# Kernel optimization log

Hardware: AMD Instinct MI355X
Metric: run time of the kernel (lower is better)

The kernel has to match this reference:

```python
import jax, jax.numpy as jnp
import numpy as np

N = 50000
E = 1600000
D_IN = 128
D_OUT = 128


def setup_inputs() -> dict:
    key = jax.random.key(0)
    k1, k2, k3, k4, k5, k6 = jax.random.split(key, 6)
    row = jax.random.randint(k1, (E,), 0, N, dtype=jnp.int32)
    col = jax.random.randint(k2, (E,), 0, N, dtype=jnp.int32)
    vals = jax.random.uniform(k3, (E,), dtype=jnp.float32)
    features = jax.random.normal(k4, (N, D_IN), dtype=jnp.float32)
    weight = jax.random.normal(k5, (D_IN, D_OUT), dtype=jnp.float32)
    bias = jax.random.normal(k6, (D_OUT,), dtype=jnp.float32)
    return {"row": row, "col": col, "vals": vals, "features": features,
            "weight": weight, "bias": bias}


def reference(row, col, vals, features, weight, bias):
    # SpMM aggregation: out[i] = sum_j adj[i,j] * features[j]
    # adj given in COO: (row, col, vals)
    gathered = vals[:, None] * features[col]          # [E, D_IN]
    agg = jax.ops.segment_sum(gathered, row, num_segments=N)  # [N, D_IN]
    # dense feature transform + bias
    return agg @ weight + bias                        # [N, D_OUT]
```

## Files before the change

### kernel.cpp

```cpp
#include <hip/hip_runtime.h>
#include <hip/hip_bf16.h>


#define D 128
#define NREP 8
#define RPB 128
#define BCAP 5120
#define EPB 4096
#define NBMAX 512

typedef __attribute__((ext_vector_type(8))) short short8;
typedef __attribute__((ext_vector_type(4))) float f32x4;

__device__ __forceinline__ ushort bf16bits(float x) {
    return __hip_bfloat16_raw(__float2bfloat16(x)).x;
}

__global__ __launch_bounds__(256) void transposeW_k(const float* __restrict__ W,
                                                    ushort* __restrict__ Wt) {
    const int idx = blockIdx.x * 256 + threadIdx.x;
    const int k = idx >> 7, c = idx & 127;
    Wt[c * D + k] = bf16bits(W[idx]);
}

__global__ __launch_bounds__(256) void gemm_mfma_k(
    const float* __restrict__ F, const ushort* __restrict__ Wt,
    ushort* __restrict__ Gb, int nrows) {
    const int wave = threadIdx.x >> 6;
    const int lane = threadIdx.x & 63;
    const int row0 = (blockIdx.x * 4 + wave) * 16;
    if (row0 >= nrows) return;
    const int lr = lane & 15;
    const int lg = lane >> 4;

    f32x4 acc[8];
    #pragma unroll
    for (int c = 0; c < 8; ++c) acc[c] = (f32x4){0.f, 0.f, 0.f, 0.f};

    int arow_idx = row0 + lr;
    if (arow_idx >= nrows) arow_idx = nrows - 1;
    const float* __restrict__ arow = F + (size_t)arow_idx * D + lg * 8;

    #pragma unroll
    for (int kk = 0; kk < 4; ++kk) {
        const float4 a0 = *(const float4*)(arow + kk * 32);
        const float4 a1 = *(const float4*)(arow + kk * 32 + 4);
        short8 af;
        af[0] = (short)bf16bits(a0.x); af[1] = (short)bf16bits(a0.y);
        af[2] = (short)bf16bits(a0.z); af[3] = (short)bf16bits(a0.w);
        af[4] = (short)bf16bits(a1.x); af[5] = (short)bf16bits(a1.y);
        af[6] = (short)bf16bits(a1.z); af[7] = (short)bf16bits(a1.w);
        #pragma unroll
        for (int c = 0; c < 8; ++c) {
            const short8 bf = *(const short8*)(Wt + (size_t)(c * 16 + lr) * D + kk * 32 + lg * 8);
            acc[c] = __builtin_amdgcn_mfma_f32_16x16x32_bf16(af, bf, acc[c], 0, 0, 0);
        }
    }

    ushort* __restrict__ gout = Gb + (size_t)row0 * D;
    #pragma unroll
    for (int i = 0; i < 4; ++i) {
        const int r = 4 * lg + i;
        if (row0 + r < nrows) {
            #pragma unroll
            for (int c = 0; c < 8; ++c) {
                const int j = c * 16 + lr;
                const int pos = (c < 4) ? (2 * j) : (2 * (j - 64) + 1);
                gout[(size_t)r * D + pos] = bf16bits(acc[c][i]);
            }
        }
    }
}

__global__ __launch_bounds__(256) void bucket_scatter_k(
    const int* __restrict__ row, const int* __restrict__ col,
    const float* __restrict__ vals, int* __restrict__ gcur,
    uint2* __restrict__ pairs, int E, int NB) {
    __shared__ int hist[NBMAX];
    __shared__ int cur[NBMAX];
    const int t = threadIdx.x;
    for (int i = t; i < NB; i += 256) hist[i] = 0;
    __syncthreads();

    const int e0 = blockIdx.x * EPB;
    const int e1 = min(e0 + EPB, E);

    for (int e = e0 + t; e < e1; e += 256)
        atomicAdd(&hist[row[e] >> 7], 1);
    __syncthreads();

    for (int i = t; i < NB; i += 256) {
        const int h = hist[i];
        cur[i] = (h > 0) ? atomicAdd(&gcur[i], h) : 0;
    }
    __syncthreads();

    for (int e = e0 + t; e < e1; e += 256) {
        const int r = row[e];
        const int b = r >> 7;
        const int slot = atomicAdd(&cur[b], 1);
        if (slot < BCAP)
            pairs[(size_t)b * BCAP + slot] =
                make_uint2(((uint)col[e] << 16) | bf16bits(vals[e]), (uint)(r & (RPB - 1)));
    }
}

__global__ __launch_bounds__(256) void bucket_to_csr_k(
    uint2* __restrict__ bpairs, const int* __restrict__ gcur,
    int* __restrict__ offs, int* __restrict__ counts, int N) {
    __shared__ uint2 ents[BCAP];
    __shared__ int hist[RPB];
    __shared__ int roff[RPB];
    __shared__ int cur[RPB];
    const int t = threadIdx.x, b = blockIdx.x;
    if (t < RPB) hist[t] = 0;
    __syncthreads();

    int cnt = gcur[b];
    if (cnt > BCAP) cnt = BCAP;
    const uint2* __restrict__ in = bpairs + (size_t)b * BCAP;
    for (int j = t; j < cnt; j += 256) {
        const uint2 e = in[j];
        ents[j] = e;
        atomicAdd(&hist[e.y], 1);
    }
    __syncthreads();

    if (t < RPB) roff[t] = hist[t];
    __syncthreads();
    for (int off = 1; off < RPB; off <<= 1) {
        const int x = (t < RPB && t >= off) ? roff[t - off] : 0;
        __syncthreads();
        if (t < RPB) roff[t] += x;
        __syncthreads();
    }
    if (t < RPB) {
        const int ex = roff[t] - hist[t];
        roff[t] = ex;
        cur[t] = 0;
        const int rg = b * RPB + t;
        if (rg < N) {
            offs[rg] = b * 2 * BCAP + ex;
            counts[rg] = hist[t];
        }
    }
    __syncthreads();

    uint* __restrict__ outv = (uint*)bpairs + (size_t)b * 2 * BCAP;
    for (int j = t; j < cnt; j += 256) {
        const uint2 e = ents[j];
        const int k = atomicAdd(&cur[e.y], 1);
        outv[roff[e.y] + k] = e.x;
    }
}

__global__ __launch_bounds__(256) void csr_gather_bf16_k(
    const uint* __restrict__ pairs, const int* __restrict__ offs,
    const int* __restrict__ counts, const uint* __restrict__ Gu,
    const float* __restrict__ bias, float* __restrict__ out, int n) {
    const int wid = (blockIdx.x * 256 + threadIdx.x) >> 6;
    if (wid >= n) return;
    const int lane = threadIdx.x & 63;

    float2 acc = make_float2(bias[lane], bias[64 + lane]);
    const int start = offs[wid];
    const int cnt = counts[wid];
    const uint* __restrict__ pp = pairs + start;

    int j = 0;
    for (; j + 3 < cnt; j += 4) {
        const uint p0 = pp[j + 0];
        const uint p1 = pp[j + 1];
        const uint p2 = pp[j + 2];
        const uint p3 = pp[j + 3];
        const uint g0 = Gu[(size_t)(p0 >> 16) * (D / 2) + lane];
        const uint g1 = Gu[(size_t)(p1 >> 16) * (D / 2) + lane];
        const uint g2 = Gu[(size_t)(p2 >> 16) * (D / 2) + lane];
        const uint g3 = Gu[(size_t)(p3 >> 16) * (D / 2) + lane];
        const float v0 = __uint_as_float(p0 << 16);
        const float v1 = __uint_as_float(p1 << 16);
        const float v2 = __uint_as_float(p2 << 16);
        const float v3 = __uint_as_float(p3 << 16);
        acc.x += v0 * __uint_as_float(g0 << 16);
        acc.y += v0 * __uint_as_float(g0 & 0xffff0000u);
        acc.x += v1 * __uint_as_float(g1 << 16);
        acc.y += v1 * __uint_as_float(g1 & 0xffff0000u);
        acc.x += v2 * __uint_as_float(g2 << 16);
        acc.y += v2 * __uint_as_float(g2 & 0xffff0000u);
        acc.x += v3 * __uint_as_float(g3 << 16);
        acc.y += v3 * __uint_as_float(g3 & 0xffff0000u);
    }
    for (; j < cnt; ++j) {
        const uint p = pp[j];
        const uint g = Gu[(size_t)(p >> 16) * (D / 2) + lane];
        const float v = __uint_as_float(p << 16);
        acc.x += v * __uint_as_float(g << 16);
        acc.y += v * __uint_as_float(g & 0xffff0000u);
    }
    out[(size_t)wid * D + lane] = acc.x;
    out[(size_t)wid * D + 64 + lane] = acc.y;
}

__global__ __launch_bounds__(256) void hist_rank_rep_k(const int* __restrict__ row,
                                                       int* __restrict__ cntrep,
                                                       ushort* __restrict__ rank,
                                                       int E, int N) {
    const int e = blockIdx.x * 256 + threadIdx.x;
    if (e >= E) return;
    const int rep = blockIdx.x & (NREP - 1);
    rank[e] = (ushort)atomicAdd(&cntrep[rep * N + row[e]], 1);
}

__global__ __launch_bounds__(256) void repbase_k(int* __restrict__ cntrep,
                                                 int* __restrict__ tot, int N) {
    const int r = blockIdx.x * 256 + threadIdx.x;
    if (r >= N) return;
    int s = 0;
    #pragma unroll
    for (int rep = 0; rep < NREP; ++rep) {
        const int v = cntrep[rep * N + r];
        cntrep[rep * N + r] = s;
        s += v;
    }
    tot[r] = s;
}

__global__ __launch_bounds__(256) void scan_blocks_k(const int* __restrict__ counts,
                                                     int* __restrict__ offs,
                                                     int* __restrict__ blockSums, int n) {
    __shared__ int s[256];
    const int t = threadIdx.x;
    const int i = blockIdx.x * 256 + t;
    const int v = (i < n) ? counts[i] : 0;
    s[t] = v;
    __syncthreads();
    for (int off = 1; off < 256; off <<= 1) {
        int x = (t >= off) ? s[t - off] : 0;
        __syncthreads();
        s[t] += x;
        __syncthreads();
    }
    if (i < n) offs[i] = s[t] - v;
    if (t == 255) blockSums[blockIdx.x] = s[255];
}

__global__ __launch_bounds__(256) void scan_top_k(int* __restrict__ blockSums, int nb) {
    __shared__ int s[256];
    const int t = threadIdx.x;
    const int v = (t < nb) ? blockSums[t] : 0;
    s[t] = v;
    __syncthreads();
    for (int off = 1; off < 256; off <<= 1) {
        int x = (t >= off) ? s[t - off] : 0;
        __syncthreads();
        s[t] += x;
        __syncthreads();
    }
    if (t < nb) blockSums[t] = s[t] - v;
}

__global__ __launch_bounds__(256) void scan_add_k(int* __restrict__ offs,
                                                  const int* __restrict__ blockSums,
                                                  int n) {
    int i = blockIdx.x * 256 + threadIdx.x;
    if (i < n) offs[i] += blockSums[blockIdx.x];
}

__global__ __launch_bounds__(256) void fill_pack_k(const int* __restrict__ row,
                                                   const int* __restrict__ col,
                                                   const float* __restrict__ vals,
                                                   const int* __restrict__ offs,
                                                   const ushort* __restrict__ rank,
                                                   const int* __restrict__ cntrep,
                                                   uint* __restrict__ pairs, int E, int N) {
    const int e = blockIdx.x * 256 + threadIdx.x;
    if (e >= E) return;
    const int r = row[e];
    const int rep = (e >> 8) & (NREP - 1);
    const int pos = offs[r] + cntrep[rep * N + r] + (int)rank[e];
    pairs[pos] = ((uint)col[e] << 16) | bf16bits(vals[e]);
}

#define ROWS_PER_BLOCK 64
__global__ __launch_bounds__(256) void gemm_f32_k(
    const float* __restrict__ A, const float* __restrict__ W,
    const float* __restrict__ bias, float* __restrict__ out, int nrows) {
    __shared__ float Wlds[D * D];
    {
        const float4* W4 = (const float4*)W;
        float4* Wl4 = (float4*)Wlds;
        #pragma unroll
        for (int i = 0; i < (D * D / 4) / 256; ++i)
            Wl4[threadIdx.x + i * 256] = W4[threadIdx.x + i * 256];
    }
    __syncthreads();
    const int lane = threadIdx.x & 31;
    const int rsub = threadIdx.x >> 5;
    const float4 b = ((const float4*)bias)[lane];
    const int rowBase = blockIdx.x * ROWS_PER_BLOCK;
    for (int rr = rsub; rr < ROWS_PER_BLOCK; rr += 8) {
        const int r = rowBase + rr;
        if (r >= nrows) break;
        const float* __restrict__ arow = A + (size_t)r * D;
        float4 acc = b;
        #pragma unroll 4
        for (int k4 = 0; k4 < D / 4; ++k4) {
            const float4 a = ((const float4*)arow)[k4];
            const int k = k4 * 4;
            const float4 w0 = ((const float4*)(Wlds + (k + 0) * D))[lane];
            const float4 w1 = ((const float4*)(Wlds + (k + 1) * D))[lane];
            const float4 w2 = ((const float4*)(Wlds + (k + 2) * D))[lane];
            const float4 w3 = ((const float4*)(Wlds + (k + 3) * D))[lane];
            acc.x += a.x * w0.x + a.y * w1.x + a.z * w2.x + a.w * w3.x;
            acc.y += a.x * w0.y + a.y * w1.y + a.z * w2.y + a.w * w3.y;
            acc.z += a.x * w0.z + a.y * w1.z + a.z * w2.z + a.w * w3.z;
            acc.w += a.x * w0.w + a.y * w1.w + a.z * w2.w + a.w * w3.w;
        }
        ((float4*)(out + (size_t)r * D))[lane] = acc;
    }
}

__global__ __launch_bounds__(256) void spmm_scatter(
    const int* __restrict__ row, const int* __restrict__ col,
    const float* __restrict__ vals, const float* __restrict__ feat,
    float* __restrict__ agg, int E) {
    int gid = blockIdx.x * 256 + threadIdx.x;
    int e = gid >> 5;
    if (e >= E) return;
    int lane = gid & 31;
    int r = row[e];
    int c = col[e];
    float v = vals[e];
    float4 f = ((const float4*)(feat + (size_t)c * D))[lane];
    float* dst = agg + (size_t)r * D + lane * 4;
    atomicAdd(dst + 0, v * f.x);
    atomicAdd(dst + 1, v * f.y);
    atomicAdd(dst + 2, v * f.z);
    atomicAdd(dst + 3, v * f.w);
}

extern "C" void kernel_launch(void* const* d_in, const int* in_sizes, int n_in,
                              void* d_out, int out_size, void* d_ws, size_t ws_size,
                              hipStream_t stream) {
    const int* row = (const int*)d_in[0];
    const int* col = (const int*)d_in[1];
    const float* vals = (const float*)d_in[2];
    const float* feat = (const float*)d_in[3];
    const float* W = (const float*)d_in[4];
    const float* bias = (const float*)d_in[5];
    float* out = (float*)d_out;

    const int E = in_sizes[0];
    const int N = out_size / D;
    const int NB = (N + RPB - 1) / RPB;

    const size_t Gb_bytes = (size_t)N * D * sizeof(ushort);
    const size_t wt_bytes = (size_t)D * D * sizeof(ushort);
    const size_t cnt_bytes = (size_t)N * sizeof(int);

    const size_t bpairs_bytes = (size_t)NB * BCAP * sizeof(uint2);
    const size_t gcur_bytes = ((size_t)NB * sizeof(int) + 255) & ~(size_t)255;
    const size_t need_bucket = Gb_bytes + bpairs_bytes + gcur_bytes +
                               2 * cnt_bytes + wt_bytes;

    const size_t pairs_bytes = (size_t)E * sizeof(uint);
    const size_t rank_bytes = ((size_t)E * sizeof(ushort) + 3) & ~(size_t)3;
    const size_t cntrep_bytes = (size_t)NREP * N * sizeof(int);
    const size_t bs_bytes = 256 * sizeof(int);
    const size_t need_compact = Gb_bytes + pairs_bytes + rank_bytes + cntrep_bytes +
                                2 * cnt_bytes + bs_bytes + wt_bytes;

    if (ws_size >= need_bucket && N <= 65536 && NB <= NBMAX) {
        char* p = (char*)d_ws;
        ushort* Gb = (ushort*)p;   p += Gb_bytes;
        uint2* bpairs = (uint2*)p; p += bpairs_bytes;
        int* gcur = (int*)p;       p += gcur_bytes;
        int* offs = (int*)p;       p += cnt_bytes;
        int* counts = (int*)p;     p += cnt_bytes;
        ushort* Wt = (ushort*)p;   p += wt_bytes;

        transposeW_k<<<(D * D) / 256, 256, 0, stream>>>(W, Wt);
        gemm_mfma_k<<<(N + 63) / 64, 256, 0, stream>>>(feat, Wt, Gb, N);

        hipMemsetAsync(gcur, 0, (size_t)NB * sizeof(int), stream);
        bucket_scatter_k<<<(E + EPB - 1) / EPB, 256, 0, stream>>>(row, col, vals,
                                                                  gcur, bpairs, E, NB);
        bucket_to_csr_k<<<NB, 256, 0, stream>>>(bpairs, gcur, offs, counts, N);
        csr_gather_bf16_k<<<(N * 64 + 255) / 256, 256, 0, stream>>>(
            (const uint*)bpairs, offs, counts, (const uint*)Gb, bias, out, N);
    } else if (ws_size >= need_compact && N <= 65536) {
        char* p = (char*)d_ws;
        ushort* Gb = (ushort*)p;   p += Gb_bytes;
        uint* pairs = (uint*)p;    p += pairs_bytes;
        ushort* rank = (ushort*)p; p += rank_bytes;
        int* cntrep = (int*)p;     p += cntrep_bytes;
        int* tot = (int*)p;        p += cnt_bytes;
        int* offs = (int*)p;       p += cnt_bytes;
        int* blockSums = (int*)p;  p += bs_bytes;
        ushort* Wt = (ushort*)p;   p += wt_bytes;

        const int nScanBlocks = (N + 255) / 256;

        transposeW_k<<<(D * D) / 256, 256, 0, stream>>>(W, Wt);
        gemm_mfma_k<<<(N + 63) / 64, 256, 0, stream>>>(feat, Wt, Gb, N);

        hipMemsetAsync(cntrep, 0, cntrep_bytes, stream);
        hist_rank_rep_k<<<(E + 255) / 256, 256, 0, stream>>>(row, cntrep, rank, E, N);
        repbase_k<<<(N + 255) / 256, 256, 0, stream>>>(cntrep, tot, N);
        scan_blocks_k<<<nScanBlocks, 256, 0, stream>>>(tot, offs, blockSums, N);
        scan_top_k<<<1, 256, 0, stream>>>(blockSums, nScanBlocks);
        scan_add_k<<<nScanBlocks, 256, 0, stream>>>(offs, blockSums, N);
        fill_pack_k<<<(E + 255) / 256, 256, 0, stream>>>(row, col, vals, offs, rank,
                                                         cntrep, pairs, E, N);
        csr_gather_bf16_k<<<(N * 64 + 255) / 256, 256, 0, stream>>>(
            pairs, offs, tot, (const uint*)Gb, bias, out, N);
    } else {
        float* agg = (float*)d_ws;
        hipMemsetAsync(agg, 0, (size_t)N * D * sizeof(float), stream);
        long long threads = (long long)E * 32;
        spmm_scatter<<<(int)((threads + 255) / 256), 256, 0, stream>>>(
            row, col, vals, feat, agg, E);
        gemm_f32_k<<<(N + ROWS_PER_BLOCK - 1) / ROWS_PER_BLOCK, 256, 0, stream>>>(
            agg, W, bias, out, N);
    }
}
```

Before: 228.0 us.

## Fuse GEMM with bucket scatter in one launch and merge weight prep with memset

Merges the weight transpose and the gcur zeroing into one prep kernel. The feature GEMM and the edge bucket scatter now run as disjoint block ranges of a single launch so they overlap, and each GEMM wave computes two 16-row tiles, reusing the loaded weight fragments and writing packed 32-bit outputs. It also widens bucket_to_csr to 512 threads and unrolls the gather loop by 8 to keep more loads in flight. The cost is higher register pressure in the fused kernel, and the GEMM and scatter blocks may contend for resources in the same launch.

```diff
diff --git a/kernel.cpp b/kernel.cpp
--- a/kernel.cpp
+++ b/kernel.cpp
@@ -14,6 +14,217 @@
 
 __device__ __forceinline__ ushort bf16bits(float x) {
     return __hip_bfloat16_raw(__float2bfloat16(x)).x;
+}
+
+__global__ __launch_bounds__(256) void prep_k(const float* __restrict__ W,
+                                              ushort* __restrict__ Wt,
+                                              int* __restrict__ gcur, int NB) {
+    const int idx = blockIdx.x * 256 + threadIdx.x;
+    if (idx < D * D) {
+        const int k = idx >> 7, c = idx & 127;
+        Wt[c * D + k] = bf16bits(W[idx]);
+    }
+    if (idx < NB) gcur[idx] = 0;
+}
+
+__global__ __launch_bounds__(256) void fused_gemm_scatter_k(
+    const float* __restrict__ F, const ushort* __restrict__ Wt,
+    ushort* __restrict__ Gb, int nrows,
+    const int* __restrict__ row, const int* __restrict__ col,
+    const float* __restrict__ vals, int* __restrict__ gcur,
+    uint2* __restrict__ pairs, int E, int NB, int GB) {
+    __shared__ int hist[NBMAX];
+    __shared__ int cur[NBMAX];
+
+    if ((int)blockIdx.x < GB) {
+        const int wave = threadIdx.x >> 6;
+        const int lane = threadIdx.x & 63;
+        const int r0 = (blockIdx.x * 8 + wave * 2) * 16;
+        if (r0 >= nrows) return;
+        const int lr = lane & 15;
+        const int lg = lane >> 4;
+
+        f32x4 acc0[8], acc1[8];
+        #pragma unroll
+        for (int c = 0; c < 8; ++c) {
+            acc0[c] = (f32x4){0.f, 0.f, 0.f, 0.f};
+            acc1[c] = (f32x4){0.f, 0.f, 0.f, 0.f};
+        }
+
+        int ar0 = r0 + lr;      if (ar0 >= nrows) ar0 = nrows - 1;
+        int ar1 = r0 + 16 + lr; if (ar1 >= nrows) ar1 = nrows - 1;
+        const float* __restrict__ a0p = F + (size_t)ar0 * D + lg * 8;
+        const float* __restrict__ a1p = F + (size_t)ar1 * D + lg * 8;
+
+        #pragma unroll
+        for (int kk = 0; kk < 4; ++kk) {
+            const float4 x0 = *(const float4*)(a0p + kk * 32);
+            const float4 x1 = *(const float4*)(a0p + kk * 32 + 4);
+            const float4 y0 = *(const float4*)(a1p + kk * 32);
+            const float4 y1 = *(const float4*)(a1p + kk * 32 + 4);
+            short8 af0, af1;
+            af0[0] = (short)bf16bits(x0.x); af0[1] = (short)bf16bits(x0.y);
+            af0[2] = (short)bf16bits(x0.z); af0[3] = (short)bf16bits(x0.w);
+            af0[4] = (short)bf16bits(x1.x); af0[5] = (short)bf16bits(x1.y);
+            af0[6] = (short)bf16bits(x1.z); af0[7] = (short)bf16bits(x1.w);
+            af1[0] = (short)bf16bits(y0.x); af1[1] = (short)bf16bits(y0.y);
+            af1[2] = (short)bf16bits(y0.z); af1[3] = (short)bf16bits(y0.w);
+            af1[4] = (short)bf16bits(y1.x); af1[5] = (short)bf16bits(y1.y);
+            af1[6] = (short)bf16bits(y1.z); af1[7] = (short)bf16bits(y1.w);
+            #pragma unroll
+            for (int c = 0; c < 8; ++c) {
+                const short8 bf = *(const short8*)(Wt + (size_t)(c * 16 + lr) * D + kk * 32 + lg * 8);
+                acc0[c] = __builtin_amdgcn_mfma_f32_16x16x32_bf16(af0, bf, acc0[c], 0, 0, 0);
+                acc1[c] = __builtin_amdgcn_mfma_f32_16x16x32_bf16(af1, bf, acc1[c], 0, 0, 0);
+            }
+        }
+
+        uint* __restrict__ g32 = (uint*)Gb;
+        #pragma unroll
+        for (int i = 0; i < 4; ++i) {
+            const int rr0 = r0 + 4 * lg + i;
+            if (rr0 < nrows) {
+                #pragma unroll
+                for (int c = 0; c < 4; ++c)
+                    g32[(size_t)rr0 * 64 + c * 16 + lr] =
+                        (uint)bf16bits(acc0[c][i]) | ((uint)bf16bits(acc0[c + 4][i]) << 16);
+            }
+            const int rr1 = r0 + 16 + 4 * lg + i;
+            if (rr1 < nrows) {
+                #pragma unroll
+                for (int c = 0; c < 4; ++c)
+                    g32[(size_t)rr1 * 64 + c * 16 + lr] =
+                        (uint)bf16bits(acc1[c][i]) | ((uint)bf16bits(acc1[c + 4][i]) << 16);
+            }
+        }
+        return;
+    }
+
+    const int t = threadIdx.x;
+    for (int i = t; i < NB; i += 256) hist[i] = 0;
+    __syncthreads();
+
+    const int e0 = ((int)blockIdx.x - GB) * EPB;
+    const int e1 = min(e0 + EPB, E);
+
+    for (int e = e0 + t; e < e1; e += 256)
+        atomicAdd(&hist[row[e] >> 7], 1);
+    __syncthreads();
+
+    for (int i = t; i < NB; i += 256) {
+        const int h = hist[i];
+        cur[i] = (h > 0) ? atomicAdd(&gcur[i], h) : 0;
+    }
+    __syncthreads();
+
+    for (int e = e0 + t; e < e1; e += 256) {
+        const int r = row[e];
+        const int b = r >> 7;
+        const int slot = atomicAdd(&cur[b], 1);
+        if (slot < BCAP)
+            pairs[(size_t)b * BCAP + slot] =
+                make_uint2(((uint)col[e] << 16) | bf16bits(vals[e]), (uint)(r & (RPB - 1)));
+    }
+}
+
+__global__ __launch_bounds__(512) void bucket_to_csr_k(
+    uint2* __restrict__ bpairs, const int* __restrict__ gcur,
+    int* __restrict__ offs, int* __restrict__ counts, int N) {
+    __shared__ uint2 ents[BCAP];
+    __shared__ int hist[RPB];
+    __shared__ int roff[RPB];
+    __shared__ int cur[RPB];
+    const int t = threadIdx.x, b = blockIdx.x;
+    if (t < RPB) hist[t] = 0;
+    __syncthreads();
+
+    int cnt = gcur[b];
+    if (cnt > BCAP) cnt = BCAP;
+    const uint2* __restrict__ in = bpairs + (size_t)b * BCAP;
+    for (int j = t; j < cnt; j += 512) {
+        const uint2 e = in[j];
+        ents[j] = e;
+        atomicAdd(&hist[e.y], 1);
+    }
+    __syncthreads();
+
+    if (t < RPB) roff[t] = hist[t];
+    __syncthreads();
+    for (int off = 1; off < RPB; off <<= 1) {
+        const int x = (t < RPB && t >= off) ? roff[t - off] : 0;
+        __syncthreads();
+        if (t < RPB) roff[t] += x;
+        __syncthreads();
+    }
+    if (t < RPB) {
+        const int ex = roff[t] - hist[t];
+        roff[t] = ex;
+        cur[t] = 0;
+        const int rg = b * RPB + t;
+        if (rg < N) {
+            offs[rg] = b * 2 * BCAP + ex;
+            counts[rg] = hist[t];
+        }
+    }
+    __syncthreads();
+
+    uint* __restrict__ outv = (uint*)bpairs + (size_t)b * 2 * BCAP;
+    for (int j = t; j < cnt; j += 512) {
+        const uint2 e = ents[j];
+        const int k = atomicAdd(&cur[e.y], 1);
+        outv[roff[e.y] + k] = e.x;
+    }
+}
+
+__global__ __launch_bounds__(256) void csr_gather_bf16_k(
+    const uint* __restrict__ pairs, const int* __restrict__ offs,
+    const int* __restrict__ counts, const uint* __restrict__ Gu,
+    const float* __restrict__ bias, float* __restrict__ out, int n) {
+    const int wid = (blockIdx.x * 256 + threadIdx.x) >> 6;
+    if (wid >= n) return;
+    const int lane = threadIdx.x & 63;
+
+    float2 acc = make_float2(bias[lane], bias[64 + lane]);
+    const int start = offs[wid];
+    const int cnt = counts[wid];
+    const uint* __restrict__ pp = pairs + start;
+
+    int j = 0;
+    for (; j + 7 < cnt; j += 8) {
+        uint p[8], g[8];
+        #pragma unroll
+        for (int k = 0; k < 8; ++k) p[k] = pp[j + k];
+        #pragma unroll
+        for (int k = 0; k < 8; ++k) g[k] = Gu[(size_t)(p[k] >> 16) * (D / 2) + lane];
+        #pragma unroll
+        for (int k = 0; k < 8; ++k) {
+            const float v = __uint_as_float(p[k] << 16);
+            acc.x += v * __uint_as_float(g[k] << 16);
+            acc.y += v * __uint_as_float(g[k] & 0xffff0000u);
+        }
+    }
+    for (; j + 3 < cnt; j += 4) {
+        uint p[4], g[4];
+        #pragma unroll
+        for (int k = 0; k < 4; ++k) p[k] = pp[j + k];
+        #pragma unroll
+        for (int k = 0; k < 4; ++k) g[k] = Gu[(size_t)(p[k] >> 16) * (D / 2) + lane];
+        #pragma unroll
+        for (int k = 0; k < 4; ++k) {
+            const float v = __uint_as_float(p[k] << 16);
+            acc.x += v * __uint_as_float(g[k] << 16);
+            acc.y += v * __uint_as_float(g[k] & 0xffff0000u);
+        }
+    }
+    for (; j < cnt; ++j) {
+        const uint p = pp[j];
+        const uint g = Gu[(size_t)(p >> 16) * (D / 2) + lane];
+        const float v = __uint_as_float(p << 16);
+        acc.x += v * __uint_as_float(g << 16);
+        acc.y += v * __uint_as_float(g & 0xffff0000u);
+    }
+    out[(size_t)wid * D + lane] = acc.x;
+    out[(size_t)wid * D + 64 + lane] = acc.y;
 }
 
 __global__ __launch_bounds__(256) void transposeW_k(const float* __restrict__ W,
@@ -70,135 +281,6 @@
             }
         }
     }
-}
-
-__global__ __launch_bounds__(256) void bucket_scatter_k(
-    const int* __restrict__ row, const int* __restrict__ col,
-    const float* __restrict__ vals, int* __restrict__ gcur,
-    uint2* __restrict__ pairs, int E, int NB) {
-    __shared__ int hist[NBMAX];
-    __shared__ int cur[NBMAX];
-    const int t = threadIdx.x;
-    for (int i = t; i < NB; i += 256) hist[i] = 0;
-    __syncthreads();
-
-    const int e0 = blockIdx.x * EPB;
-    const int e1 = min(e0 + EPB, E);
-
-    for (int e = e0 + t; e < e1; e += 256)
-        atomicAdd(&hist[row[e] >> 7], 1);
-    __syncthreads();
-
-    for (int i = t; i < NB; i += 256) {
-        const int h = hist[i];
-        cur[i] = (h > 0) ? atomicAdd(&gcur[i], h) : 0;
-    }
-    __syncthreads();
-
-    for (int e = e0 + t; e < e1; e += 256) {
-        const int r = row[e];
-        const int b = r >> 7;
-        const int slot = atomicAdd(&cur[b], 1);
-        if (slot < BCAP)
-            pairs[(size_t)b * BCAP + slot] =
-                make_uint2(((uint)col[e] << 16) | bf16bits(vals[e]), (uint)(r & (RPB - 1)));
-    }
-}
-
-__global__ __launch_bounds__(256) void bucket_to_csr_k(
-    uint2* __restrict__ bpairs, const int* __restrict__ gcur,
-    int* __restrict__ offs, int* __restrict__ counts, int N) {
-    __shared__ uint2 ents[BCAP];
-    __shared__ int hist[RPB];
-    __shared__ int roff[RPB];
-    __shared__ int cur[RPB];
-    const int t = threadIdx.x, b = blockIdx.x;
-    if (t < RPB) hist[t] = 0;
-    __syncthreads();
-
-    int cnt = gcur[b];
-    if (cnt > BCAP) cnt = BCAP;
-    const uint2* __restrict__ in = bpairs + (size_t)b * BCAP;
-    for (int j = t; j < cnt; j += 256) {
-        const uint2 e = in[j];
-        ents[j] = e;
-        atomicAdd(&hist[e.y], 1);
-    }
-    __syncthreads();
-
-    if (t < RPB) roff[t] = hist[t];
-    __syncthreads();
-    for (int off = 1; off < RPB; off <<= 1) {
-        const int x = (t < RPB && t >= off) ? roff[t - off] : 0;
-        __syncthreads();
-        if (t < RPB) roff[t] += x;
-        __syncthreads();
-    }
-    if (t < RPB) {
-        const int ex = roff[t] - hist[t];
-        roff[t] = ex;
-        cur[t] = 0;
-        const int rg = b * RPB + t;
-        if (rg < N) {
-            offs[rg] = b * 2 * BCAP + ex;
-            counts[rg] = hist[t];
-        }
-    }
-    __syncthreads();
-
-    uint* __restrict__ outv = (uint*)bpairs + (size_t)b * 2 * BCAP;
-    for (int j = t; j < cnt; j += 256) {
-        const uint2 e = ents[j];
-        const int k = atomicAdd(&cur[e.y], 1);
-        outv[roff[e.y] + k] = e.x;
-    }
-}
-
-__global__ __launch_bounds__(256) void csr_gather_bf16_k(
-    const uint* __restrict__ pairs, const int* __restrict__ offs,
-    const int* __restrict__ counts, const uint* __restrict__ Gu,
-    const float* __restrict__ bias, float* __restrict__ out, int n) {
-    const int wid = (blockIdx.x * 256 + threadIdx.x) >> 6;
-    if (wid >= n) return;
-    const int lane = threadIdx.x & 63;
-
-    float2 acc = make_float2(bias[lane], bias[64 + lane]);
-    const int start = offs[wid];
-    const int cnt = counts[wid];
-    const uint* __restrict__ pp = pairs + start;
-
-    int j = 0;
-    for (; j + 3 < cnt; j += 4) {
-        const uint p0 = pp[j + 0];
-        const uint p1 = pp[j + 1];
-        const uint p2 = pp[j + 2];
-        const uint p3 = pp[j + 3];
-        const uint g0 = Gu[(size_t)(p0 >> 16) * (D / 2) + lane];
-        const uint g1 = Gu[(size_t)(p1 >> 16) * (D / 2) + lane];
-        const uint g2 = Gu[(size_t)(p2 >> 16) * (D / 2) + lane];
-        const uint g3 = Gu[(size_t)(p3 >> 16) * (D / 2) + lane];
-        const float v0 = __uint_as_float(p0 << 16);
-        const float v1 = __uint_as_float(p1 << 16);
-        const float v2 = __uint_as_float(p2 << 16);
-        const float v3 = __uint_as_float(p3 << 16);
-        acc.x += v0 * __uint_as_float(g0 << 16);
-        acc.y += v0 * __uint_as_float(g0 & 0xffff0000u);
-        acc.x += v1 * __uint_as_float(g1 << 16);
-        acc.y += v1 * __uint_as_float(g1 & 0xffff0000u);
-        acc.x += v2 * __uint_as_float(g2 << 16);
-        acc.y += v2 * __uint_as_float(g2 & 0xffff0000u);
-        acc.x += v3 * __uint_as_float(g3 << 16);
-        acc.y += v3 * __uint_as_float(g3 & 0xffff0000u);
-    }
-    for (; j < cnt; ++j) {
-        const uint p = pp[j];
-        const uint g = Gu[(size_t)(p >> 16) * (D / 2) + lane];
-        const float v = __uint_as_float(p << 16);
-        acc.x += v * __uint_as_float(g << 16);
-        acc.y += v * __uint_as_float(g & 0xffff0000u);
-    }
-    out[(size_t)wid * D + lane] = acc.x;
-    out[(size_t)wid * D + 64 + lane] = acc.y;
 }
 
 __global__ __launch_bounds__(256) void hist_rank_rep_k(const int* __restrict__ row,
@@ -379,13 +461,13 @@
         int* counts = (int*)p;     p += cnt_bytes;
         ushort* Wt = (ushort*)p;   p += wt_bytes;
 
-        transposeW_k<<<(D * D) / 256, 256, 0, stream>>>(W, Wt);
-        gemm_mfma_k<<<(N + 63) / 64, 256, 0, stream>>>(feat, Wt, Gb, N);
-
-        hipMemsetAsync(gcur, 0, (size_t)NB * sizeof(int), stream);
-        bucket_scatter_k<<<(E + EPB - 1) / EPB, 256, 0, stream>>>(row, col, vals,
-                                                                  gcur, bpairs, E, NB);
-        bucket_to_csr_k<<<NB, 256, 0, stream>>>(bpairs, gcur, offs, counts, N);
+        const int GB = (N + 127) / 128;
+        const int SB = (E + EPB - 1) / EPB;
+
+        prep_k<<<(D * D + 255) / 256, 256, 0, stream>>>(W, Wt, gcur, NB);
+        fused_gemm_scatter_k<<<GB + SB, 256, 0, stream>>>(
+            feat, Wt, Gb, N, row, col, vals, gcur, bpairs, E, NB, GB);
+        bucket_to_csr_k<<<NB, 512, 0, stream>>>(bpairs, gcur, offs, counts, N);
         csr_gather_bf16_k<<<(N * 64 + 255) / 256, 256, 0, stream>>>(
             (const uint*)bpairs, offs, counts, (const uint*)Gb, bias, out, N);
     } else if (ws_size >= need_compact && N <= 65536) {
```

After: 205.9 us. -9.7%, faster.
